# Kernel tuning notes

Measured on AMD Instinct MI355X. Metric: run time of the kernel, lower is better.

The kernel has to match this reference:

```python
import jax, jax.numpy as jnp
import numpy as np

N = 32768      # total nodes (2048 graphs * 16 nodes)
E = 491520     # total edges (2048 graphs * 16*15)
F = 11         # in_node_nf
H = 64         # hidden_nf
G = 2048       # number of graphs
NN = 16        # nodes per graph
R = 1024       # n_reactions
L = 4          # n_layers
EIN = 2 * H + 1        # edge_mlp input: [h[row], h[col], radial]
NIN = H + H + F        # node_mlp input: [h, agg, node_attr=h0]


def setup_inputs() -> dict:
    key = jax.random.key(0)
    ks = jax.random.split(key, 24)
    s = 0.05
    d = {
        "h0": jax.random.normal(ks[0], (N, F), jnp.float32),
        "positions": jax.random.normal(ks[1], (N, 3), jnp.float32),
        "edges": jax.random.randint(ks[2], (2, E), 0, N),
        "node_mask": jnp.ones((N, 1), jnp.float32),
        "edge_mask": jnp.ones((E, 1), jnp.float32),
        "reaction_indexes": jax.random.randint(ks[3], (G,), 0, R),
        "reaction_signs": jax.random.normal(ks[4], (G,), jnp.float32),
        # params
        "emb_w": jax.random.normal(ks[5], (F, H), jnp.float32) * s,
        "emb_b": jnp.zeros((H,), jnp.float32),
        "edge_w1": jax.random.normal(ks[6], (L, EIN, H), jnp.float32) * s,
        "edge_b1": jnp.zeros((L, H), jnp.float32),
        "edge_w2": jax.random.normal(ks[7], (L, H, H), jnp.float32) * s,
        "edge_b2": jnp.zeros((L, H), jnp.float32),
        "node_w1": jax.random.normal(ks[8], (L, NIN, H), jnp.float32) * s,
        "node_b1": jnp.zeros((L, H), jnp.float32),
        "node_w2": jax.random.normal(ks[9], (L, H, H), jnp.float32) * s,
        "node_b2": jnp.zeros((L, H), jnp.float32),
        "dec_w1": jax.random.normal(ks[10], (H, H), jnp.float32) * s,
        "dec_b1": jnp.zeros((H,), jnp.float32),
        "dec_w2": jax.random.normal(ks[11], (H, H), jnp.float32) * s,
        "dec_b2": jnp.zeros((H,), jnp.float32),
        "g_w1": jax.random.normal(ks[12], (H, H), jnp.float32) * s,
        "g_b1": jnp.zeros((H,), jnp.float32),
        "g_w2": jax.random.normal(ks[13], (H, 1), jnp.float32) * s,
        "g_b2": jnp.zeros((1,), jnp.float32),
        "n_nodes": NN,
        "n_reactions": R,
    }
    return d


def reference(h0, positions, edges, node_mask, edge_mask, reaction_indexes,
              reaction_signs, emb_w, emb_b, edge_w1, edge_b1, edge_w2, edge_b2,
              node_w1, node_b1, node_w2, node_b2, dec_w1, dec_b1, dec_w2,
              dec_b2, g_w1, g_b1, g_w2, g_b2, n_nodes, n_reactions):
    silu = jax.nn.silu
    row, col = edges[0], edges[1]
    n = h0.shape[0]

    # radial is constant across layers (coords never updated in this variant)
    coord_diff = positions[row] - positions[col]          # [E, 3]
    radial = jnp.sum(coord_diff ** 2, axis=1, keepdims=True)  # [E, 1]

    h = h0 @ emb_w + emb_b                                # [N, H]
    for i in range(edge_w1.shape[0]):
        # edge model
        e_in = jnp.concatenate([h[row], h[col], radial], axis=1)  # [E, 2H+1]
        e = silu(e_in @ edge_w1[i] + edge_b1[i])
        e = silu(e @ edge_w2[i] + edge_b2[i])             # [E, H]
        e = e * edge_mask
        # scatter-sum aggregation by source node
        agg = jax.ops.segment_sum(e, row, num_segments=n)  # [N, H]
        # node model (node_attr = h0)
        n_in = jnp.concatenate([h, agg, h0], axis=1)      # [N, 2H+F]
        h = silu(n_in @ node_w1[i] + node_b1[i]) @ node_w2[i] + node_b2[i]

    # node decoder
    h = silu(h @ dec_w1 + dec_b1) @ dec_w2 + dec_b2
    h = h * node_mask
    # pool per graph (fixed n_nodes per graph)
    hg = h.reshape(-1, n_nodes, h.shape[-1]).sum(axis=1)  # [G, H]
    # graph decoder
    temp = silu(hg @ g_w1 + g_b1) @ g_w2 + g_b2           # [G, 1]
    # signed per-reaction aggregation
    pred = jnp.zeros((n_reactions,), h.dtype).at[reaction_indexes].add(
        temp[:, 0] * reaction_signs)
    return pred
```

## Files before the change

### kernel.cpp

```cpp
#include <hip/hip_runtime.h>
#include <math.h>
#include <stdint.h>

#define N_NODES 32768
#define N_EDGES 491520
#define F_IN    11
#define H       64
#define G_GRAPHS 2048
#define NN_PER_G 16
#define R_REACT 1024
#define L_LAYERS 4
#define EIN     129
#define NIN     139
#define NPBLK   32

#define WPROJ 0
#define WE2   65536
#define WN1   98304
#define WN2   180224
#define WD1   212992
#define WD2   221184
#define WTOT  229376

typedef __attribute__((ext_vector_type(8))) short short8;
typedef __attribute__((ext_vector_type(4))) float f32x4;

__device__ __forceinline__ float silu_f(float x) {
    return x * __builtin_amdgcn_rcpf(1.0f + __expf(-x));
}
__device__ __forceinline__ void atomAddF(float* p, float v) {
    unsafeAtomicAdd(p, v);
}
__device__ __forceinline__ float bf2f(unsigned short b) {
    union { float f; unsigned u; } v; v.u = ((unsigned)b) << 16;
    return v.f;
}
__device__ __forceinline__ unsigned short f2bf(float x) {
    union { float f; unsigned u; } v; v.f = x;
    unsigned r = v.u + 0x7FFFu + ((v.u >> 16) & 1u);
    return (unsigned short)(r >> 16);
}
__device__ __forceinline__ void splitbf(float x, unsigned short& hi, unsigned short& lo) {
    hi = f2bf(x);
    lo = f2bf(x - bf2f(hi));
}
__device__ __forceinline__ void splitbf_t(float x, unsigned short& hi, unsigned short& lo) {
    union { float f; unsigned u; } v; v.f = x;
    hi = (unsigned short)(v.u >> 16);
    union { float f; unsigned u; } w; w.f = x - bf2f(hi);
    lo = (unsigned short)(w.u >> 16);
}

__global__ __launch_bounds__(64) void k_prepw(
        const float* __restrict__ ew1, const float* __restrict__ ew2,
        const float* __restrict__ nw1, const float* __restrict__ nw2,
        const float* __restrict__ dw1, const float* __restrict__ dw2,
        short* __restrict__ wsW) {
    const int b = blockIdx.x;
    const int lane = threadIdx.x;
    const int quad = lane >> 4, m16 = lane & 15;
    short8 h8, l8;
    short* base; int fidx, half;

    if (b < 64) {
        int l = b >> 4, f = b & 15;
        int nt = f >> 1, kf = f & 1;
#pragma unroll
        for (int j = 0; j < 8; ++j) {
            int row = (nt >= 4 ? 64 : 0) + kf * 32 + quad * 8 + j;
            unsigned short hi, lo;
            splitbf(ew1[l * EIN * H + row * H + (nt & 3) * 16 + m16], hi, lo);
            h8[j] = (short)hi; l8[j] = (short)lo;
        }
        base = wsW + WPROJ + l * 16384; fidx = f; half = 8192;
    } else if (b < 96) {
        int bb = b - 64; int l = bb >> 3, f = bb & 7;
        int nt = f >> 1, kf = f & 1;
#pragma unroll
        for (int j = 0; j < 8; ++j) {
            int row = kf * 32 + quad * 8 + j;
            unsigned short hi, lo;
            splitbf(ew2[l * H * H + row * H + nt * 16 + m16], hi, lo);
            h8[j] = (short)hi; l8[j] = (short)lo;
        }
        base = wsW + WE2 + l * 8192; fidx = f; half = 4096;
    } else if (b < 176) {
        int bb = b - 96; int l = bb / 20, f = bb % 20;
        int nt = f / 5, kf = f % 5;
#pragma unroll
        for (int j = 0; j < 8; ++j) {
            int row = kf * 32 + quad * 8 + j;
            float w = (row < NIN) ? nw1[l * NIN * H + row * H + nt * 16 + m16] : 0.0f;
            unsigned short hi, lo; splitbf(w, hi, lo);
            h8[j] = (short)hi; l8[j] = (short)lo;
        }
        base = wsW + WN1 + l * 20480; fidx = f; half = 10240;
    } else if (b < 208) {
        int bb = b - 176; int l = bb >> 3, f = bb & 7;
        int nt = f >> 1, kf = f & 1;
#pragma unroll
        for (int j = 0; j < 8; ++j) {
            int row = kf * 32 + quad * 8 + j;
            unsigned short hi, lo;
            splitbf(nw2[l * H * H + row * H + nt * 16 + m16], hi, lo);
            h8[j] = (short)hi; l8[j] = (short)lo;
        }
        base = wsW + WN2 + l * 8192; fidx = f; half = 4096;
    } else if (b < 216) {
        int f = b - 208;
        int nt = f >> 1, kf = f & 1;
#pragma unroll
        for (int j = 0; j < 8; ++j) {
            int row = kf * 32 + quad * 8 + j;
            unsigned short hi, lo;
            splitbf(dw1[row * H + nt * 16 + m16], hi, lo);
            h8[j] = (short)hi; l8[j] = (short)lo;
        }
        base = wsW + WD1; fidx = f; half = 4096;
    } else {
        int f = b - 216;
        int nt = f >> 1, kf = f & 1;
#pragma unroll
        for (int j = 0; j < 8; ++j) {
            int row = kf * 32 + quad * 8 + j;
            unsigned short hi, lo;
            splitbf(dw2[row * H + nt * 16 + m16], hi, lo);
            h8[j] = (short)hi; l8[j] = (short)lo;
        }
        base = wsW + WD2; fidx = f; half = 4096;
    }
    *(short8*)(base + (fidx * 64 + lane) * 8) = h8;
    *(short8*)(base + half + (fidx * 64 + lane) * 8) = l8;
}

__global__ __launch_bounds__(256) void k_embed(
        const float* __restrict__ h0, const float* __restrict__ emb_w,
        const float* __restrict__ emb_b, float* __restrict__ h) {
    int tid = blockIdx.x * 256 + threadIdx.x;
    int n = tid >> 6, j = tid & 63;
    float acc = emb_b[j];
#pragma unroll
    for (int k = 0; k < F_IN; ++k)
        acc += h0[n * F_IN + k] * emb_w[k * H + j];
    h[tid] = acc;
}

__global__ __launch_bounds__(256) void k_radial(
        const int* __restrict__ edges, const float* __restrict__ pos,
        float* __restrict__ radial) {
    int e = blockIdx.x * 256 + threadIdx.x;
    int r = edges[e], c = edges[N_EDGES + e];
    float dx = pos[r * 3 + 0] - pos[c * 3 + 0];
    float dy = pos[r * 3 + 1] - pos[c * 3 + 1];
    float dz = pos[r * 3 + 2] - pos[c * 3 + 2];
    radial[e] = dx * dx + dy * dy + dz * dz;
}

__global__ __launch_bounds__(256) void k_hist(
        const int* __restrict__ edges, int* __restrict__ deg) {
    int e = blockIdx.x * 256 + threadIdx.x;
    atomicAdd(&deg[edges[e]], 1);
}

__global__ __launch_bounds__(128) void k_scan_blk(
        const int* __restrict__ deg, int* __restrict__ off,
        int* __restrict__ bsum) {
    __shared__ int sd[128];
    int b = blockIdx.x;
    sd[threadIdx.x] = deg[b * 128 + threadIdx.x];
    __syncthreads();
    if (threadIdx.x == 0) {
        int s = 0;
        for (int i = 0; i < 128; ++i) { int d = sd[i]; sd[i] = s; s += d; }
        bsum[b] = s;
    }
    __syncthreads();
    off[b * 128 + threadIdx.x] = sd[threadIdx.x];
}

__global__ __launch_bounds__(256) void k_scan_top(
        const int* __restrict__ bsum, int* __restrict__ bbase) {
    __shared__ int sb[256];
    sb[threadIdx.x] = bsum[threadIdx.x];
    __syncthreads();
    if (threadIdx.x == 0) {
        int s = 0;
        for (int i = 0; i < 256; ++i) { int d = sb[i]; sb[i] = s; s += d; }
    }
    __syncthreads();
    bbase[threadIdx.x] = sb[threadIdx.x];
}

__global__ __launch_bounds__(256) void k_cursor(
        const int* __restrict__ off, const int* __restrict__ bbase,
        int* __restrict__ nstart, int* __restrict__ cursor) {
    int n = blockIdx.x * 256 + threadIdx.x;
    int ns = off[n] + bbase[n >> 7];
    nstart[n] = ns;
    cursor[n] = ns;
    if (n == 0) nstart[N_NODES] = N_EDGES;
}

__global__ __launch_bounds__(256) void k_fill(
        const int* __restrict__ edges, const float* __restrict__ radial,
        const float* __restrict__ emask, int* __restrict__ cursor,
        int* __restrict__ csrP, float* __restrict__ csrR,
        float* __restrict__ csrM) {
    int e = blockIdx.x * 256 + threadIdx.x;
    int r = edges[e];
    int pos = atomicAdd(&cursor[r], 1);
    csrP[pos] = edges[N_EDGES + e] | ((r & (NPBLK - 1)) << 16);
    csrR[pos] = radial[e];
    csrM[pos] = emask[e];
}

__global__ __launch_bounds__(64, 2) void k_nodeproj_m(
        const float* __restrict__ h, const short* __restrict__ wP,
        const float* __restrict__ b1,
        float* __restrict__ PA, float* __restrict__ PB) {
    const int lane = threadIdx.x;
    const int quad = lane >> 4, m16 = lane & 15;
    const int nb = blockIdx.x * 16;

    const float* hp = h + (nb + m16) * H + quad * 8;
    float av[16];
    *(float4*)&av[0]  = *(const float4*)(hp + 0);
    *(float4*)&av[4]  = *(const float4*)(hp + 4);
    *(float4*)&av[8]  = *(const float4*)(hp + 32);
    *(float4*)&av[12] = *(const float4*)(hp + 36);
    float b1v[4];
#pragma unroll
    for (int nt = 0; nt < 4; ++nt) b1v[nt] = b1[nt * 16 + m16];

    short8 Ah0, Ah1, Al0, Al1;
#pragma unroll
    for (int j = 0; j < 8; ++j) {
        unsigned short hi, lo;
        splitbf_t(av[j], hi, lo);     Ah0[j] = (short)hi; Al0[j] = (short)lo;
        splitbf_t(av[8 + j], hi, lo); Ah1[j] = (short)hi; Al1[j] = (short)lo;
    }
#pragma unroll
    for (int nt = 0; nt < 8; ++nt) {
        short8 bh0 = *(const short8*)(wP + ((nt*2+0) * 64 + lane) * 8);
        short8 bh1 = *(const short8*)(wP + ((nt*2+1) * 64 + lane) * 8);
        short8 bl0 = *(const short8*)(wP + 8192 + ((nt*2+0) * 64 + lane) * 8);
        short8 bl1 = *(const short8*)(wP + 8192 + ((nt*2+1) * 64 + lane) * 8);
        f32x4 a = {0.0f, 0.0f, 0.0f, 0.0f};
        a = __builtin_amdgcn_mfma_f32_16x16x32_bf16(Ah0, bh0, a, 0, 0, 0);
        a = __builtin_amdgcn_mfma_f32_16x16x32_bf16(Ah1, bh1, a, 0, 0, 0);
        a = __builtin_amdgcn_mfma_f32_16x16x32_bf16(Ah0, bl0, a, 0, 0, 0);
        a = __builtin_amdgcn_mfma_f32_16x16x32_bf16(Ah1, bl1, a, 0, 0, 0);
        a = __builtin_amdgcn_mfma_f32_16x16x32_bf16(Al0, bh0, a, 0, 0, 0);
        a = __builtin_amdgcn_mfma_f32_16x16x32_bf16(Al1, bh1, a, 0, 0, 0);
#pragma unroll
        for (int r4 = 0; r4 < 4; ++r4) {
            const int node = nb + quad * 4 + r4;
            if (nt < 4)
                PA[node * H + nt * 16 + m16] = a[r4] + b1v[nt];
            else
                PB[node * H + (nt - 4) * 16 + m16] = a[r4];
        }
    }
}

__global__ __launch_bounds__(256, 2) void k_edge6(
        const float* __restrict__ PA, const float* __restrict__ PB,
        const int* __restrict__ nstart, const int* __restrict__ csrP,
        const float* __restrict__ csrR, const float* __restrict__ csrM,
        const float* __restrict__ W1,
        const short* __restrict__ wE2, const float* __restrict__ b2,
        float* __restrict__ agg) {
    const int tid = threadIdx.x;
    const int lane = tid & 63, wave = tid >> 6;
    const int quad = lane >> 4, m16 = lane & 15;
    const int n0 = blockIdx.x * NPBLK;

    __shared__ float aggld[NPBLK * 68];
    for (int i = tid; i < NPBLK * 68; i += 256) aggld[i] = 0.0f;

    short8 Bh[8], Bl[8];
#pragma unroll
    for (int f = 0; f < 8; ++f) {
        Bh[f] = *(const short8*)(wE2 + (f * 64 + lane) * 8);
        Bl[f] = *(const short8*)(wE2 + 4096 + (f * 64 + lane) * 8);
    }
    float w1cr[16];
#pragma unroll
    for (int i = 0; i < 16; ++i) {
        int k = (i < 8) ? (quad * 8 + i) : (32 + quad * 8 + (i - 8));
        w1cr[i] = W1[128 * H + k];
    }
    float b2v[4];
#pragma unroll
    for (int nt = 0; nt < 4; ++nt) b2v[nt] = b2[nt * 16 + m16];

    const int start = nstart[n0];
    const int end   = nstart[n0 + NPBLK];
    __syncthreads();

    const int ntiles = (end - start + 15) >> 4;

    int   pkA = 0, pkB = 0;
    float radA = 0.0f, radB = 0.0f;
    float avA[16], bvA[16];

    int tA = wave;
    bool haveA = tA < ntiles;
    if (haveA) {
        const int idx = start + tA * 16 + m16;
        const int ss  = min(idx, N_EDGES - 1);
        pkA  = csrP[ss];
        radA = csrR[ss];
        const int c  = pkA & 0xFFFF;
        const int rl = pkA >> 16;
        const float* par = PA + (n0 + rl) * H + quad * 8;
        const float* pbr = PB + c * H + quad * 8;
        *(float4*)&avA[0]  = *(const float4*)(par + 0);
        *(float4*)&avA[4]  = *(const float4*)(par + 4);
        *(float4*)&avA[8]  = *(const float4*)(par + 32);
        *(float4*)&avA[12] = *(const float4*)(par + 36);
        *(float4*)&bvA[0]  = *(const float4*)(pbr + 0);
        *(float4*)&bvA[4]  = *(const float4*)(pbr + 4);
        *(float4*)&bvA[8]  = *(const float4*)(pbr + 32);
        *(float4*)&bvA[12] = *(const float4*)(pbr + 36);
    }
    int tB = tA + 4;
    bool haveB = tB < ntiles;
    if (haveB) {
        const int idx = start + tB * 16 + m16;
        const int ss  = min(idx, N_EDGES - 1);
        pkB  = csrP[ss];
        radB = csrR[ss];
    }

    while (haveA) {
        float bvB[16];
        if (haveB) {
            const int c = pkB & 0xFFFF;
            const float* pbr = PB + c * H + quad * 8;
            *(float4*)&bvB[0]  = *(const float4*)(pbr + 0);
            *(float4*)&bvB[4]  = *(const float4*)(pbr + 4);
            *(float4*)&bvB[8]  = *(const float4*)(pbr + 32);
            *(float4*)&bvB[12] = *(const float4*)(pbr + 36);
        }
        const int tC = tB + 4;
        const bool haveC = tC < ntiles;
        int pkC = 0; float radC = 0.0f;
        if (haveC) {
            const int idx = start + tC * 16 + m16;
            const int ss  = min(idx, N_EDGES - 1);
            pkC  = csrP[ss];
            radC = csrR[ss];
        }
        int rlq[4]; float mkq[4];
        const int sb = start + tA * 16 + quad * 4;
#pragma unroll
        for (int r4 = 0; r4 < 4; ++r4) {
            int s = sb + r4, s2 = min(s, N_EDGES - 1);
            rlq[r4] = csrP[s2] >> 16;
            mkq[r4] = (s < end) ? csrM[s2] : 0.0f;
        }

        short8 Ah0, Ah1, Al0, Al1;
#pragma unroll
        for (int i = 0; i < 8; ++i) {
            unsigned short hi, lo;
            splitbf_t(silu_f(avA[i] + bvA[i] + radA * w1cr[i]), hi, lo);
            Ah0[i] = (short)hi; Al0[i] = (short)lo;
            splitbf_t(silu_f(avA[8+i] + bvA[8+i] + radA * w1cr[8+i]), hi, lo);
            Ah1[i] = (short)hi; Al1[i] = (short)lo;
        }
        f32x4 acc[4];
#pragma unroll
        for (int nt = 0; nt < 4; ++nt) {
            f32x4 a = {0.0f, 0.0f, 0.0f, 0.0f};
            a = __builtin_amdgcn_mfma_f32_16x16x32_bf16(Ah0, Bh[nt*2+0], a, 0, 0, 0);
            a = __builtin_amdgcn_mfma_f32_16x16x32_bf16(Ah1, Bh[nt*2+1], a, 0, 0, 0);
            a = __builtin_amdgcn_mfma_f32_16x16x32_bf16(Ah0, Bl[nt*2+0], a, 0, 0, 0);
            a = __builtin_amdgcn_mfma_f32_16x16x32_bf16(Ah1, Bl[nt*2+1], a, 0, 0, 0);
            a = __builtin_amdgcn_mfma_f32_16x16x32_bf16(Al0, Bh[nt*2+0], a, 0, 0, 0);
            a = __builtin_amdgcn_mfma_f32_16x16x32_bf16(Al1, Bh[nt*2+1], a, 0, 0, 0);
            acc[nt] = a;
        }

#pragma unroll
        for (int nt = 0; nt < 4; ++nt) {
            float oo[4];
#pragma unroll
            for (int r4 = 0; r4 < 4; ++r4)
                oo[r4] = silu_f(acc[nt][r4] + b2v[nt]) * mkq[r4];
            int cur = rlq[0]; float s = oo[0];
#pragma unroll
            for (int r4 = 1; r4 < 4; ++r4) {
                if (rlq[r4] == cur) { s += oo[r4]; }
                else {
                    atomicAdd(&aggld[cur * 68 + nt * 16 + m16], s);
                    cur = rlq[r4]; s = oo[r4];
                }
            }
            atomicAdd(&aggld[cur * 68 + nt * 16 + m16], s);
        }

        if (haveB) {
            const int rl = pkB >> 16;
            const float* par = PA + (n0 + rl) * H + quad * 8;
            *(float4*)&avA[0]  = *(const float4*)(par + 0);
            *(float4*)&avA[4]  = *(const float4*)(par + 4);
            *(float4*)&avA[8]  = *(const float4*)(par + 32);
            *(float4*)&avA[12] = *(const float4*)(par + 36);
#pragma unroll
            for (int i = 0; i < 16; ++i) bvA[i] = bvB[i];
            pkA = pkB; radA = radB;
        }
        pkB = pkC; radB = radC;
        tA = tB; tB = tC; haveA = haveB; haveB = haveC;
    }

    __syncthreads();
#pragma unroll
    for (int i = tid; i < NPBLK * 16; i += 256) {
        int n = i >> 4, cb = (i & 15) << 2;
        *(float4*)&agg[(n0 + n) * H + cb] = *(const float4*)&aggld[n * 68 + cb];
    }
}

__global__ __launch_bounds__(64, 2) void k_node_m(
        float* __restrict__ h, const float* __restrict__ agg,
        const float* __restrict__ h0,
        const short* __restrict__ wN1, const float* __restrict__ b1,
        const short* __restrict__ wN2, const float* __restrict__ b2) {
    const int lane = threadIdx.x;
    const int quad = lane >> 4, m16 = lane & 15;
    const int nb = blockIdx.x * 16;

    float b1v[4], b2v[4];
#pragma unroll
    for (int nt = 0; nt < 4; ++nt) {
        b1v[nt] = b1[nt * 16 + m16];
        b2v[nt] = b2[nt * 16 + m16];
    }

    __shared__ float tld[16 * 68];

    float a1[5][8];
    const float* hp = h + (nb + m16) * H + quad * 8;
    const float* ap = agg + (nb + m16) * H + quad * 8;
    *(float4*)&a1[0][0] = *(const float4*)(hp + 0);
    *(float4*)&a1[0][4] = *(const float4*)(hp + 4);
    *(float4*)&a1[1][0] = *(const float4*)(hp + 32);
    *(float4*)&a1[1][4] = *(const float4*)(hp + 36);
    *(float4*)&a1[2][0] = *(const float4*)(ap + 0);
    *(float4*)&a1[2][4] = *(const float4*)(ap + 4);
    *(float4*)&a1[3][0] = *(const float4*)(ap + 32);
    *(float4*)&a1[3][4] = *(const float4*)(ap + 36);
    const float* h0p = h0 + (nb + m16) * F_IN;
#pragma unroll
    for (int j = 0; j < 8; ++j) {
        int kk = quad * 8 + j;
        a1[4][j] = (kk < F_IN) ? h0p[kk] : 0.0f;
    }
    short8 A1h[5], A1l[5];
#pragma unroll
    for (int kf = 0; kf < 5; ++kf) {
        short8 ah, al;
#pragma unroll
        for (int j = 0; j < 8; ++j) {
            unsigned short hi, lo; splitbf_t(a1[kf][j], hi, lo);
            ah[j] = (short)hi; al[j] = (short)lo;
        }
        A1h[kf] = ah; A1l[kf] = al;
    }
#pragma unroll
    for (int nt = 0; nt < 4; ++nt) {
        short8 bh[5], bl[5];
#pragma unroll
        for (int kf = 0; kf < 5; ++kf) {
            bh[kf] = *(const short8*)(wN1 + ((nt*5+kf) * 64 + lane) * 8);
            bl[kf] = *(const short8*)(wN1 + 10240 + ((nt*5+kf) * 64 + lane) * 8);
        }
        f32x4 a = {0.0f, 0.0f, 0.0f, 0.0f};
#pragma unroll
        for (int kf = 0; kf < 5; ++kf)
            a = __builtin_amdgcn_mfma_f32_16x16x32_bf16(A1h[kf], bh[kf], a, 0, 0, 0);
#pragma unroll
        for (int kf = 0; kf < 5; ++kf)
            a = __builtin_amdgcn_mfma_f32_16x16x32_bf16(A1h[kf], bl[kf], a, 0, 0, 0);
#pragma unroll
        for (int kf = 0; kf < 5; ++kf)
            a = __builtin_amdgcn_mfma_f32_16x16x32_bf16(A1l[kf], bh[kf], a, 0, 0, 0);
#pragma unroll
        for (int r4 = 0; r4 < 4; ++r4)
            tld[(quad * 4 + r4) * 68 + nt * 16 + m16] = silu_f(a[r4] + b1v[nt]);
    }
    __syncthreads();
    float a2[16];
    *(float4*)&a2[0]  = *(const float4*)&tld[m16 * 68 + quad * 8 + 0];
    *(float4*)&a2[4]  = *(const float4*)&tld[m16 * 68 + quad * 8 + 4];
    *(float4*)&a2[8]  = *(const float4*)&tld[m16 * 68 + quad * 8 + 32];
    *(float4*)&a2[12] = *(const float4*)&tld[m16 * 68 + quad * 8 + 36];
    short8 A2h0, A2h1, A2l0, A2l1;
#pragma unroll
    for (int j = 0; j < 8; ++j) {
        unsigned short hi, lo;
        splitbf_t(a2[j], hi, lo);     A2h0[j] = (short)hi; A2l0[j] = (short)lo;
        splitbf_t(a2[8+j], hi, lo);   A2h1[j] = (short)hi; A2l1[j] = (short)lo;
    }
#pragma unroll
    for (int nt = 0; nt < 4; ++nt) {
        short8 bh0 = *(const short8*)(wN2 + ((nt*2+0) * 64 + lane) * 8);
        short8 bh1 = *(const short8*)(wN2 + ((nt*2+1) * 64 + lane) * 8);
        short8 bl0 = *(const short8*)(wN2 + 4096 + ((nt*2+0) * 64 + lane) * 8);
        short8 bl1 = *(const short8*)(wN2 + 4096 + ((nt*2+1) * 64 + lane) * 8);
        f32x4 a = {0.0f, 0.0f, 0.0f, 0.0f};
        a = __builtin_amdgcn_mfma_f32_16x16x32_bf16(A2h0, bh0, a, 0, 0, 0);
        a = __builtin_amdgcn_mfma_f32_16x16x32_bf16(A2h1, bh1, a, 0, 0, 0);
        a = __builtin_amdgcn_mfma_f32_16x16x32_bf16(A2h0, bl0, a, 0, 0, 0);
        a = __builtin_amdgcn_mfma_f32_16x16x32_bf16(A2h1, bl1, a, 0, 0, 0);
        a = __builtin_amdgcn_mfma_f32_16x16x32_bf16(A2l0, bh0, a, 0, 0, 0);
        a = __builtin_amdgcn_mfma_f32_16x16x32_bf16(A2l1, bh1, a, 0, 0, 0);
#pragma unroll
        for (int r4 = 0; r4 < 4; ++r4) {
            const int node = nb + quad * 4 + r4;
            h[node * H + nt * 16 + m16] = a[r4] + b2v[nt];
        }
    }
}

__global__ __launch_bounds__(64, 2) void k_dec_m(
        float* __restrict__ h, const float* __restrict__ nmask,
        const short* __restrict__ wD1, const float* __restrict__ b1,
        const short* __restrict__ wD2, const float* __restrict__ b2) {
    const int lane = threadIdx.x;
    const int quad = lane >> 4, m16 = lane & 15;
    const int nb = blockIdx.x * 16;

    float b1v[4], b2v[4];
#pragma unroll
    for (int nt = 0; nt < 4; ++nt) {
        b1v[nt] = b1[nt * 16 + m16];
        b2v[nt] = b2[nt * 16 + m16];
    }
    __shared__ float tld[16 * 68];

    const float* hp = h + (nb + m16) * H + quad * 8;
    float av[16];
    *(float4*)&av[0]  = *(const float4*)(hp + 0);
    *(float4*)&av[4]  = *(const float4*)(hp + 4);
    *(float4*)&av[8]  = *(const float4*)(hp + 32);
    *(float4*)&av[12] = *(const float4*)(hp + 36);
    short8 Ah0, Ah1, Al0, Al1;
#pragma unroll
    for (int j = 0; j < 8; ++j) {
        unsigned short hi, lo;
        splitbf_t(av[j], hi, lo);     Ah0[j] = (short)hi; Al0[j] = (short)lo;
        splitbf_t(av[8+j], hi, lo);   Ah1[j] = (short)hi; Al1[j] = (short)lo;
    }
#pragma unroll
    for (int nt = 0; nt < 4; ++nt) {
        short8 bh0 = *(const short8*)(wD1 + ((nt*2+0) * 64 + lane) * 8);
        short8 bh1 = *(const short8*)(wD1 + ((nt*2+1) * 64 + lane) * 8);
        short8 bl0 = *(const short8*)(wD1 + 4096 + ((nt*2+0) * 64 + lane) * 8);
        short8 bl1 = *(const short8*)(wD1 + 4096 + ((nt*2+1) * 64 + lane) * 8);
        f32x4 a = {0.0f, 0.0f, 0.0f, 0.0f};
        a = __builtin_amdgcn_mfma_f32_16x16x32_bf16(Ah0, bh0, a, 0, 0, 0);
        a = __builtin_amdgcn_mfma_f32_16x16x32_bf16(Ah1, bh1, a, 0, 0, 0);
        a = __builtin_amdgcn_mfma_f32_16x16x32_bf16(Ah0, bl0, a, 0, 0, 0);
        a = __builtin_amdgcn_mfma_f32_16x16x32_bf16(Ah1, bl1, a, 0, 0, 0);
        a = __builtin_amdgcn_mfma_f32_16x16x32_bf16(Al0, bh0, a, 0, 0, 0);
        a = __builtin_amdgcn_mfma_f32_16x16x32_bf16(Al1, bh1, a, 0, 0, 0);
#pragma unroll
        for (int r4 = 0; r4 < 4; ++r4)
            tld[(quad * 4 + r4) * 68 + nt * 16 + m16] = silu_f(a[r4] + b1v[nt]);
    }
    __syncthreads();
    float a2[16];
    *(float4*)&a2[0]  = *(const float4*)&tld[m16 * 68 + quad * 8 + 0];
    *(float4*)&a2[4]  = *(const float4*)&tld[m16 * 68 + quad * 8 + 4];
    *(float4*)&a2[8]  = *(const float4*)&tld[m16 * 68 + quad * 8 + 32];
    *(float4*)&a2[12] = *(const float4*)&tld[m16 * 68 + quad * 8 + 36];
    short8 A2h0, A2h1, A2l0, A2l1;
#pragma unroll
    for (int j = 0; j < 8; ++j) {
        unsigned short hi, lo;
        splitbf_t(a2[j], hi, lo);     A2h0[j] = (short)hi; A2l0[j] = (short)lo;
        splitbf_t(a2[8+j], hi, lo);   A2h1[j] = (short)hi; A2l1[j] = (short)lo;
    }
#pragma unroll
    for (int nt = 0; nt < 4; ++nt) {
        short8 bh0 = *(const short8*)(wD2 + ((nt*2+0) * 64 + lane) * 8);
        short8 bh1 = *(const short8*)(wD2 + ((nt*2+1) * 64 + lane) * 8);
        short8 bl0 = *(const short8*)(wD2 + 4096 + ((nt*2+0) * 64 + lane) * 8);
        short8 bl1 = *(const short8*)(wD2 + 4096 + ((nt*2+1) * 64 + lane) * 8);
        f32x4 a = {0.0f, 0.0f, 0.0f, 0.0f};
        a = __builtin_amdgcn_mfma_f32_16x16x32_bf16(A2h0, bh0, a, 0, 0, 0);
        a = __builtin_amdgcn_mfma_f32_16x16x32_bf16(A2h1, bh1, a, 0, 0, 0);
        a = __builtin_amdgcn_mfma_f32_16x16x32_bf16(A2h0, bl0, a, 0, 0, 0);
        a = __builtin_amdgcn_mfma_f32_16x16x32_bf16(A2h1, bl1, a, 0, 0, 0);
        a = __builtin_amdgcn_mfma_f32_16x16x32_bf16(A2l0, bh0, a, 0, 0, 0);
        a = __builtin_amdgcn_mfma_f32_16x16x32_bf16(A2l1, bh1, a, 0, 0, 0);
#pragma unroll
        for (int r4 = 0; r4 < 4; ++r4) {
            const int node = nb + quad * 4 + r4;
            const float nm = nmask[node];
            h[node * H + nt * 16 + m16] = (a[r4] + b2v[nt]) * nm;
        }
    }
}

__global__ __launch_bounds__(64) void k_graph(
        const float* __restrict__ h, const int* __restrict__ rid,
        const float* __restrict__ rsign,
        const float* __restrict__ W1, const float* __restrict__ b1,
        const float* __restrict__ W2, const float* __restrict__ b2,
        float* __restrict__ pred) {
    const int g = blockIdx.x;
    const int lane = threadIdx.x;
    float hgv = 0.0f;
#pragma unroll
    for (int m = 0; m < NN_PER_G; ++m)
        hgv += h[(g * NN_PER_G + m) * H + lane];
    __shared__ __align__(16) float hgs[64];
    hgs[lane] = hgv;
    __syncthreads();
    float acc = b1[lane];
#pragma unroll
    for (int k = 0; k < H; ++k)
        acc += hgs[k] * W1[k * H + lane];
    float part = silu_f(acc) * W2[lane];
#pragma unroll
    for (int off = 32; off > 0; off >>= 1)
        part += __shfl_down(part, off);
    if (lane == 0)
        atomAddF(&pred[rid[g]], (part + b2[0]) * rsign[g]);
}

extern "C" void kernel_launch(void* const* d_in, const int* in_sizes, int n_in,
                              void* d_out, int out_size, void* d_ws, size_t ws_size,
                              hipStream_t stream) {
    const float* h0      = (const float*)d_in[0];
    const float* pos     = (const float*)d_in[1];
    const int*   edges   = (const int*)d_in[2];
    const float* nmask   = (const float*)d_in[3];
    const float* emask   = (const float*)d_in[4];
    const int*   rid     = (const int*)d_in[5];
    const float* rsign   = (const float*)d_in[6];
    const float* emb_w   = (const float*)d_in[7];
    const float* emb_b   = (const float*)d_in[8];
    const float* edge_w1 = (const float*)d_in[9];
    const float* edge_b1 = (const float*)d_in[10];
    const float* edge_w2 = (const float*)d_in[11];
    const float* edge_b2 = (const float*)d_in[12];
    const float* node_w1 = (const float*)d_in[13];
    const float* node_b1 = (const float*)d_in[14];
    const float* node_w2 = (const float*)d_in[15];
    const float* node_b2 = (const float*)d_in[16];
    const float* dec_w1  = (const float*)d_in[17];
    const float* dec_b1  = (const float*)d_in[18];
    const float* dec_w2  = (const float*)d_in[19];
    const float* dec_b2  = (const float*)d_in[20];
    const float* g_w1    = (const float*)d_in[21];
    const float* g_b1    = (const float*)d_in[22];
    const float* g_w2    = (const float*)d_in[23];
    const float* g_b2    = (const float*)d_in[24];

    float* h      = (float*)d_ws;
    float* agg    = h + N_NODES * H;
    float* radial = agg + N_NODES * H;
    float* PA     = radial + N_EDGES;
    float* PB     = PA + N_NODES * H;
    float* csrR   = PB + N_NODES * H;
    float* csrM   = csrR + N_EDGES;
    int*   csrP   = (int*)(csrM + N_EDGES);
    int*   deg    = csrP + N_EDGES;
    int*   off    = deg + N_NODES;
    int*   bsum   = off + N_NODES;
    int*   bbase  = bsum + 256;
    int*   nstart = bbase + 256;
    int*   cursor = nstart + N_NODES + 1;
    short* wsW    = (short*)((((uintptr_t)(cursor + N_NODES)) + 255) & ~(uintptr_t)255);
    float* pred   = (float*)d_out;

    hipMemsetAsync(d_out, 0, R_REACT * sizeof(float), stream);
    hipMemsetAsync(deg, 0, N_NODES * sizeof(int), stream);

    k_prepw<<<224, 64, 0, stream>>>(edge_w1, edge_w2, node_w1, node_w2,
                                    dec_w1, dec_w2, wsW);
    k_embed<<<(N_NODES * H) / 256, 256, 0, stream>>>(h0, emb_w, emb_b, h);
    k_radial<<<N_EDGES / 256, 256, 0, stream>>>(edges, pos, radial);
    k_hist<<<N_EDGES / 256, 256, 0, stream>>>(edges, deg);
    k_scan_blk<<<256, 128, 0, stream>>>(deg, off, bsum);
    k_scan_top<<<1, 256, 0, stream>>>(bsum, bbase);
    k_cursor<<<N_NODES / 256, 256, 0, stream>>>(off, bbase, nstart, cursor);
    k_fill<<<N_EDGES / 256, 256, 0, stream>>>(edges, radial, emask, cursor,
                                              csrP, csrR, csrM);

    for (int i = 0; i < L_LAYERS; ++i) {
        k_nodeproj_m<<<N_NODES / 16, 64, 0, stream>>>(
            h, wsW + WPROJ + i * 16384, edge_b1 + i * H, PA, PB);
        k_edge6<<<N_NODES / NPBLK, 256, 0, stream>>>(
            PA, PB, nstart, csrP, csrR, csrM,
            edge_w1 + i * EIN * H,
            wsW + WE2 + i * 8192, edge_b2 + i * H, agg);
        k_node_m<<<N_NODES / 16, 64, 0, stream>>>(
            h, agg, h0,
            wsW + WN1 + i * 20480, node_b1 + i * H,
            wsW + WN2 + i * 8192,  node_b2 + i * H);
    }
    k_dec_m<<<N_NODES / 16, 64, 0, stream>>>(h, nmask, wsW + WD1, dec_b1,
                                             wsW + WD2, dec_b2);
    k_graph<<<G_GRAPHS, 64, 0, stream>>>(h, rid, rsign, g_w1, g_b1, g_w2,
                                         g_b2, pred);
}
```

Measured before the change: 524.9 us.

## Fuse embed, node MLP, edge projection, decoder and graph pooling into fewer kernels

Folds the embedding into an MFMA kernel that also computes the first edge projection, and folds the node MLP of each layer together with the next layer's edge projection. The last layer's node MLP is merged with the node decoder, the per-graph pooling and the graph MLP, and radial computation moves into the CSR fill kernel. The aim is to cut kernel launches and the global round trips of h and radial. NPBLK also drops from 32 to 16, which doubles the edge kernel's block count, and the merged kernels use more registers and extra barriers.

```diff
diff --git a/kernel.cpp b/kernel.cpp
--- a/kernel.cpp
+++ b/kernel.cpp
@@ -12,7 +12,7 @@
 #define L_LAYERS 4
 #define EIN     129
 #define NIN     139
-#define NPBLK   32
+#define NPBLK   16
 
 #define WPROJ 0
 #define WE2   65536
@@ -20,7 +20,8 @@
 #define WN2   180224
 #define WD1   212992
 #define WD2   221184
-#define WTOT  229376
+#define WEMB  229376
+#define WTOT  233472
 
 typedef __attribute__((ext_vector_type(8))) short short8;
 typedef __attribute__((ext_vector_type(4))) float f32x4;
@@ -55,6 +56,7 @@
         const float* __restrict__ ew1, const float* __restrict__ ew2,
         const float* __restrict__ nw1, const float* __restrict__ nw2,
         const float* __restrict__ dw1, const float* __restrict__ dw2,
+        const float* __restrict__ embw,
         short* __restrict__ wsW) {
     const int b = blockIdx.x;
     const int lane = threadIdx.x;
@@ -117,7 +119,7 @@
             h8[j] = (short)hi; l8[j] = (short)lo;
         }
         base = wsW + WD1; fidx = f; half = 4096;
-    } else {
+    } else if (b < 224) {
         int f = b - 216;
         int nt = f >> 1, kf = f & 1;
 #pragma unroll
@@ -128,32 +130,19 @@
             h8[j] = (short)hi; l8[j] = (short)lo;
         }
         base = wsW + WD2; fidx = f; half = 4096;
+    } else {
+        int f = b - 224;
+#pragma unroll
+        for (int j = 0; j < 8; ++j) {
+            int row = quad * 8 + j;
+            float w = (row < F_IN) ? embw[row * H + f * 16 + m16] : 0.0f;
+            unsigned short hi, lo; splitbf(w, hi, lo);
+            h8[j] = (short)hi; l8[j] = (short)lo;
+        }
+        base = wsW + WEMB; fidx = f; half = 2048;
     }
     *(short8*)(base + (fidx * 64 + lane) * 8) = h8;
     *(short8*)(base + half + (fidx * 64 + lane) * 8) = l8;
-}
-
-__global__ __launch_bounds__(256) void k_embed(
-        const float* __restrict__ h0, const float* __restrict__ emb_w,
-        const float* __restrict__ emb_b, float* __restrict__ h) {
-    int tid = blockIdx.x * 256 + threadIdx.x;
-    int n = tid >> 6, j = tid & 63;
-    float acc = emb_b[j];
-#pragma unroll
-    for (int k = 0; k < F_IN; ++k)
-        acc += h0[n * F_IN + k] * emb_w[k * H + j];
-    h[tid] = acc;
-}
-
-__global__ __launch_bounds__(256) void k_radial(
-        const int* __restrict__ edges, const float* __restrict__ pos,
-        float* __restrict__ radial) {
-    int e = blockIdx.x * 256 + threadIdx.x;
-    int r = edges[e], c = edges[N_EDGES + e];
-    float dx = pos[r * 3 + 0] - pos[c * 3 + 0];
-    float dy = pos[r * 3 + 1] - pos[c * 3 + 1];
-    float dz = pos[r * 3 + 2] - pos[c * 3 + 2];
-    radial[e] = dx * dx + dy * dy + dz * dz;
 }
 
 __global__ __launch_bounds__(256) void k_hist(
@@ -202,36 +191,71 @@
 }
 
 __global__ __launch_bounds__(256) void k_fill(
-        const int* __restrict__ edges, const float* __restrict__ radial,
+        const int* __restrict__ edges, const float* __restrict__ posi,
         const float* __restrict__ emask, int* __restrict__ cursor,
         int* __restrict__ csrP, float* __restrict__ csrR,
         float* __restrict__ csrM) {
     int e = blockIdx.x * 256 + threadIdx.x;
-    int r = edges[e];
-    int pos = atomicAdd(&cursor[r], 1);
-    csrP[pos] = edges[N_EDGES + e] | ((r & (NPBLK - 1)) << 16);
-    csrR[pos] = radial[e];
-    csrM[pos] = emask[e];
-}
-
-__global__ __launch_bounds__(64, 2) void k_nodeproj_m(
-        const float* __restrict__ h, const short* __restrict__ wP,
-        const float* __restrict__ b1,
-        float* __restrict__ PA, float* __restrict__ PB) {
+    int r = edges[e], c = edges[N_EDGES + e];
+    float dx = posi[r * 3 + 0] - posi[c * 3 + 0];
+    float dy = posi[r * 3 + 1] - posi[c * 3 + 1];
+    float dz = posi[r * 3 + 2] - posi[c * 3 + 2];
+    float rad = dx * dx + dy * dy + dz * dz;
+    int p = atomicAdd(&cursor[r], 1);
+    csrP[p] = c | ((r & (NPBLK - 1)) << 16);
+    csrR[p] = rad;
+    csrM[p] = emask[e];
+}
+
+__global__ __launch_bounds__(64, 2) void k_embed_proj(
+        const float* __restrict__ h0, const short* __restrict__ wEmb,
+        const float* __restrict__ emb_b,
+        const short* __restrict__ wP, const float* __restrict__ eb1,
+        float* __restrict__ h, float* __restrict__ PA, float* __restrict__ PB) {
     const int lane = threadIdx.x;
     const int quad = lane >> 4, m16 = lane & 15;
     const int nb = blockIdx.x * 16;
-
-    const float* hp = h + (nb + m16) * H + quad * 8;
+    __shared__ float tld[16 * 68];
+
+    float a0[8];
+    const float* h0p = h0 + (nb + m16) * F_IN;
+#pragma unroll
+    for (int j = 0; j < 8; ++j) {
+        int kk = quad * 8 + j;
+        a0[j] = (kk < F_IN) ? h0p[kk] : 0.0f;
+    }
+    short8 A0h, A0l;
+#pragma unroll
+    for (int j = 0; j < 8; ++j) {
+        unsigned short hi, lo; splitbf_t(a0[j], hi, lo);
+        A0h[j] = (short)hi; A0l[j] = (short)lo;
+    }
+    float ebv[4];
+#pragma unroll
+    for (int nt = 0; nt < 4; ++nt) ebv[nt] = emb_b[nt * 16 + m16];
+
+#pragma unroll
+    for (int nt = 0; nt < 4; ++nt) {
+        short8 bh = *(const short8*)(wEmb + (nt * 64 + lane) * 8);
+        short8 bl = *(const short8*)(wEmb + 2048 + (nt * 64 + lane) * 8);
+        f32x4 a = {0.0f, 0.0f, 0.0f, 0.0f};
+        a = __builtin_amdgcn_mfma_f32_16x16x32_bf16(A0h, bh, a, 0, 0, 0);
+        a = __builtin_amdgcn_mfma_f32_16x16x32_bf16(A0h, bl, a, 0, 0, 0);
+        a = __builtin_amdgcn_mfma_f32_16x16x32_bf16(A0l, bh, a, 0, 0, 0);
+#pragma unroll
+        for (int r4 = 0; r4 < 4; ++r4) {
+            const int node = nb + quad * 4 + r4;
+            float hv = a[r4] + ebv[nt];
+            h[node * H + nt * 16 + m16] = hv;
+            tld[(quad * 4 + r4) * 68 + nt * 16 + m16] = hv;
+        }
+    }
+    __syncthreads();
     float av[16];
-    *(float4*)&av[0]  = *(const float4*)(hp + 0);
-    *(float4*)&av[4]  = *(const float4*)(hp + 4);
-    *(float4*)&av[8]  = *(const float4*)(hp + 32);
-    *(float4*)&av[12] = *(const float4*)(hp + 36);
-    float b1v[4];
-#pragma unroll
-    for (int nt = 0; nt < 4; ++nt) b1v[nt] = b1[nt * 16 + m16];
-
+    *(float4*)&av[0]  = *(const float4*)&tld[m16 * 68 + quad * 8 + 0];
+    *(float4*)&av[4]  = *(const float4*)&tld[m16 * 68 + quad * 8 + 4];
+    *(float4*)&av[8]  = *(const float4*)&tld[m16 * 68 + quad * 8 + 32];
+    *(float4*)&av[12] = *(const float4*)&tld[m16 * 68 + quad * 8 + 36];
     short8 Ah0, Ah1, Al0, Al1;
 #pragma unroll
     for (int j = 0; j < 8; ++j) {
@@ -239,6 +263,9 @@
         splitbf_t(av[j], hi, lo);     Ah0[j] = (short)hi; Al0[j] = (short)lo;
         splitbf_t(av[8 + j], hi, lo); Ah1[j] = (short)hi; Al1[j] = (short)lo;
     }
+    float b1v[4];
+#pragma unroll
+    for (int nt = 0; nt < 4; ++nt) b1v[nt] = eb1[nt * 16 + m16];
 #pragma unroll
     for (int nt = 0; nt < 8; ++nt) {
         short8 bh0 = *(const short8*)(wP + ((nt*2+0) * 64 + lane) * 8);
@@ -424,11 +451,13 @@
     }
 }
 
-__global__ __launch_bounds__(64, 2) void k_node_m(
+__global__ __launch_bounds__(64, 2) void k_node_proj(
         float* __restrict__ h, const float* __restrict__ agg,
         const float* __restrict__ h0,
         const short* __restrict__ wN1, const float* __restrict__ b1,
-        const short* __restrict__ wN2, const float* __restrict__ b2) {
+        const short* __restrict__ wN2, const float* __restrict__ b2,
+        const short* __restrict__ wPn, const float* __restrict__ eb1n,
+        float* __restrict__ PA, float* __restrict__ PB) {
     const int lane = threadIdx.x;
     const int quad = lane >> 4, m16 = lane & 15;
     const int nb = blockIdx.x * 16;
@@ -439,7 +468,6 @@
         b1v[nt] = b1[nt * 16 + m16];
         b2v[nt] = b2[nt * 16 + m16];
     }
-
     __shared__ float tld[16 * 68];
 
     float a1[5][8];
@@ -505,6 +533,7 @@
         splitbf_t(a2[j], hi, lo);     A2h0[j] = (short)hi; A2l0[j] = (short)lo;
         splitbf_t(a2[8+j], hi, lo);   A2h1[j] = (short)hi; A2l1[j] = (short)lo;
     }
+    __syncthreads();
 #pragma unroll
     for (int nt = 0; nt < 4; ++nt) {
         short8 bh0 = *(const short8*)(wN2 + ((nt*2+0) * 64 + lane) * 8);
@@ -521,53 +550,128 @@
 #pragma unroll
         for (int r4 = 0; r4 < 4; ++r4) {
             const int node = nb + quad * 4 + r4;
-            h[node * H + nt * 16 + m16] = a[r4] + b2v[nt];
-        }
-    }
-}
-
-__global__ __launch_bounds__(64, 2) void k_dec_m(
-        float* __restrict__ h, const float* __restrict__ nmask,
-        const short* __restrict__ wD1, const float* __restrict__ b1,
-        const short* __restrict__ wD2, const float* __restrict__ b2) {
+            float hv = a[r4] + b2v[nt];
+            h[node * H + nt * 16 + m16] = hv;
+            tld[(quad * 4 + r4) * 68 + nt * 16 + m16] = hv;
+        }
+    }
+    __syncthreads();
+    float av[16];
+    *(float4*)&av[0]  = *(const float4*)&tld[m16 * 68 + quad * 8 + 0];
+    *(float4*)&av[4]  = *(const float4*)&tld[m16 * 68 + quad * 8 + 4];
+    *(float4*)&av[8]  = *(const float4*)&tld[m16 * 68 + quad * 8 + 32];
+    *(float4*)&av[12] = *(const float4*)&tld[m16 * 68 + quad * 8 + 36];
+    short8 Ph0, Ph1, Pl0, Pl1;
+#pragma unroll
+    for (int j = 0; j < 8; ++j) {
+        unsigned short hi, lo;
+        splitbf_t(av[j], hi, lo);     Ph0[j] = (short)hi; Pl0[j] = (short)lo;
+        splitbf_t(av[8+j], hi, lo);   Ph1[j] = (short)hi; Pl1[j] = (short)lo;
+    }
+    float b1ev[4];
+#pragma unroll
+    for (int nt = 0; nt < 4; ++nt) b1ev[nt] = eb1n[nt * 16 + m16];
+#pragma unroll
+    for (int nt = 0; nt < 8; ++nt) {
+        short8 bh0 = *(const short8*)(wPn + ((nt*2+0) * 64 + lane) * 8);
+        short8 bh1 = *(const short8*)(wPn + ((nt*2+1) * 64 + lane) * 8);
+        short8 bl0 = *(const short8*)(wPn + 8192 + ((nt*2+0) * 64 + lane) * 8);
+        short8 bl1 = *(const short8*)(wPn + 8192 + ((nt*2+1) * 64 + lane) * 8);
+        f32x4 a = {0.0f, 0.0f, 0.0f, 0.0f};
+        a = __builtin_amdgcn_mfma_f32_16x16x32_bf16(Ph0, bh0, a, 0, 0, 0);
+        a = __builtin_amdgcn_mfma_f32_16x16x32_bf16(Ph1, bh1, a, 0, 0, 0);
+        a = __builtin_amdgcn_mfma_f32_16x16x32_bf16(Ph0, bl0, a, 0, 0, 0);
+        a = __builtin_amdgcn_mfma_f32_16x16x32_bf16(Ph1, bl1, a, 0, 0, 0);
+        a = __builtin_amdgcn_mfma_f32_16x16x32_bf16(Pl0, bh0, a, 0, 0, 0);
+        a = __builtin_amdgcn_mfma_f32_16x16x32_bf16(Pl1, bh1, a, 0, 0, 0);
+#pragma unroll
+        for (int r4 = 0; r4 < 4; ++r4) {
+            const int node = nb + quad * 4 + r4;
+            if (nt < 4)
+                PA[node * H + nt * 16 + m16] = a[r4] + b1ev[nt];
+            else
+                PB[node * H + (nt - 4) * 16 + m16] = a[r4];
+        }
+    }
+}
+
+__global__ __launch_bounds__(64, 2) void k_node_dec_graph(
+        const float* __restrict__ h, const float* __restrict__ agg,
+        const float* __restrict__ h0,
+        const short* __restrict__ wN1, const float* __restrict__ b1,
+        const short* __restrict__ wN2, const float* __restrict__ b2,
+        const short* __restrict__ wD1, const float* __restrict__ db1,
+        const short* __restrict__ wD2, const float* __restrict__ db2,
+        const float* __restrict__ nmask,
+        const float* __restrict__ gW1, const float* __restrict__ gb1,
+        const float* __restrict__ gW2, const float* __restrict__ gb2,
+        const int* __restrict__ rid, const float* __restrict__ rsign,
+        float* __restrict__ pred) {
     const int lane = threadIdx.x;
     const int quad = lane >> 4, m16 = lane & 15;
     const int nb = blockIdx.x * 16;
 
-    float b1v[4], b2v[4];
+    float b1v[4], b2v[4], db1v[4], db2v[4];
 #pragma unroll
     for (int nt = 0; nt < 4; ++nt) {
-        b1v[nt] = b1[nt * 16 + m16];
-        b2v[nt] = b2[nt * 16 + m16];
-    }
+        b1v[nt]  = b1[nt * 16 + m16];
+        b2v[nt]  = b2[nt * 16 + m16];
+        db1v[nt] = db1[nt * 16 + m16];
+        db2v[nt] = db2[nt * 16 + m16];
+    }
+    float nm[4];
+#pragma unroll
+    for (int r4 = 0; r4 < 4; ++r4) nm[r4] = nmask[nb + quad * 4 + r4];
+
     __shared__ float tld[16 * 68];
-
+    __shared__ __align__(16) float hgs[64];
+
+    float a1[5][8];
     const float* hp = h + (nb + m16) * H + quad * 8;
-    float av[16];
-    *(float4*)&av[0]  = *(const float4*)(hp + 0);
-    *(float4*)&av[4]  = *(const float4*)(hp + 4);
-    *(float4*)&av[8]  = *(const float4*)(hp + 32);
-    *(float4*)&av[12] = *(const float4*)(hp + 36);
-    short8 Ah0, Ah1, Al0, Al1;
-#pragma unroll
-    for (int j = 0; j < 8; ++j) {
-        unsigned short hi, lo;
-        splitbf_t(av[j], hi, lo);     Ah0[j] = (short)hi; Al0[j] = (short)lo;
-        splitbf_t(av[8+j], hi, lo);   Ah1[j] = (short)hi; Al1[j] = (short)lo;
+    const float* ap = agg + (nb + m16) * H + quad * 8;
+    *(float4*)&a1[0][0] = *(const float4*)(hp + 0);
+    *(float4*)&a1[0][4] = *(const float4*)(hp + 4);
+    *(float4*)&a1[1][0] = *(const float4*)(hp + 32);
+    *(float4*)&a1[1][4] = *(const float4*)(hp + 36);
+    *(float4*)&a1[2][0] = *(const float4*)(ap + 0);
+    *(float4*)&a1[2][4] = *(const float4*)(ap + 4);
+    *(float4*)&a1[3][0] = *(const float4*)(ap + 32);
+    *(float4*)&a1[3][4] = *(const float4*)(ap + 36);
+    const float* h0p = h0 + (nb + m16) * F_IN;
+#pragma unroll
+    for (int j = 0; j < 8; ++j) {
+        int kk = quad * 8 + j;
+        a1[4][j] = (kk < F_IN) ? h0p[kk] : 0.0f;
+    }
+    short8 A1h[5], A1l[5];
+#pragma unroll
+    for (int kf = 0; kf < 5; ++kf) {
+        short8 ah, al;
+#pragma unroll
+        for (int j = 0; j < 8; ++j) {
+            unsigned short hi, lo; splitbf_t(a1[kf][j], hi, lo);
+            ah[j] = (short)hi; al[j] = (short)lo;
+        }
+        A1h[kf] = ah; A1l[kf] = al;
     }
 #pragma unroll
     for (int nt = 0; nt < 4; ++nt) {
-        short8 bh0 = *(const short8*)(wD1 + ((nt*2+0) * 64 + lane) * 8);
-        short8 bh1 = *(const short8*)(wD1 + ((nt*2+1) * 64 + lane) * 8);
-        short8 bl0 = *(const short8*)(wD1 + 4096 + ((nt*2+0) * 64 + lane) * 8);
-        short8 bl1 = *(const short8*)(wD1 + 4096 + ((nt*2+1) * 64 + lane) * 8);
+        short8 bh[5], bl[5];
+#pragma unroll
+        for (int kf = 0; kf < 5; ++kf) {
+            bh[kf] = *(const short8*)(wN1 + ((nt*5+kf) * 64 + lane) * 8);
+            bl[kf] = *(const short8*)(wN1 + 10240 + ((nt*5+kf) * 64 + lane) * 8);
+        }
         f32x4 a = {0.0f, 0.0f, 0.0f, 0.0f};
-        a = __builtin_amdgcn_mfma_f32_16x16x32_bf16(Ah0, bh0, a, 0, 0, 0);
-        a = __builtin_amdgcn_mfma_f32_16x16x32_bf16(Ah1, bh1, a, 0, 0, 0);
-        a = __builtin_amdgcn_mfma_f32_16x16x32_bf16(Ah0, bl0, a, 0, 0, 0);
-        a = __builtin_amdgcn_mfma_f32_16x16x32_bf16(Ah1, bl1, a, 0, 0, 0);
-        a = __builtin_amdgcn_mfma_f32_16x16x32_bf16(Al0, bh0, a, 0, 0, 0);
-        a = __builtin_amdgcn_mfma_f32_16x16x32_bf16(Al1, bh1, a, 0, 0, 0);
+#pragma unroll
+        for (int kf = 0; kf < 5; ++kf)
+            a = __builtin_amdgcn_mfma_f32_16x16x32_bf16(A1h[kf], bh[kf], a, 0, 0, 0);
+#pragma unroll
+        for (int kf = 0; kf < 5; ++kf)
+            a = __builtin_amdgcn_mfma_f32_16x16x32_bf16(A1h[kf], bl[kf], a, 0, 0, 0);
+#pragma unroll
+        for (int kf = 0; kf < 5; ++kf)
+            a = __builtin_amdgcn_mfma_f32_16x16x32_bf16(A1l[kf], bh[kf], a, 0, 0, 0);
 #pragma unroll
         for (int r4 = 0; r4 < 4; ++r4)
             tld[(quad * 4 + r4) * 68 + nt * 16 + m16] = silu_f(a[r4] + b1v[nt]);
@@ -585,12 +689,13 @@
         splitbf_t(a2[j], hi, lo);     A2h0[j] = (short)hi; A2l0[j] = (short)lo;
         splitbf_t(a2[8+j], hi, lo);   A2h1[j] = (short)hi; A2l1[j] = (short)lo;
     }
+    __syncthreads();
 #pragma unroll
     for (int nt = 0; nt < 4; ++nt) {
-        short8 bh0 = *(const short8*)(wD2 + ((nt*2+0) * 64 + lane) * 8);
-        short8 bh1 = *(const short8*)(wD2 + ((nt*2+1) * 64 + lane) * 8);
-        short8 bl0 = *(const short8*)(wD2 + 4096 + ((nt*2+0) * 64 + lane) * 8);
-        short8 bl1 = *(const short8*)(wD2 + 4096 + ((nt*2+1) * 64 + lane) * 8);
+        short8 bh0 = *(const short8*)(wN2 + ((nt*2+0) * 64 + lane) * 8);
+        short8 bh1 = *(const short8*)(wN2 + ((nt*2+1) * 64 + lane) * 8);
+        short8 bl0 = *(const short8*)(wN2 + 4096 + ((nt*2+0) * 64 + lane) * 8);
+        short8 bl1 = *(const short8*)(wN2 + 4096 + ((nt*2+1) * 64 + lane) * 8);
         f32x4 a = {0.0f, 0.0f, 0.0f, 0.0f};
         a = __builtin_amdgcn_mfma_f32_16x16x32_bf16(A2h0, bh0, a, 0, 0, 0);
         a = __builtin_amdgcn_mfma_f32_16x16x32_bf16(A2h1, bh1, a, 0, 0, 0);
@@ -599,39 +704,85 @@
         a = __builtin_amdgcn_mfma_f32_16x16x32_bf16(A2l0, bh0, a, 0, 0, 0);
         a = __builtin_amdgcn_mfma_f32_16x16x32_bf16(A2l1, bh1, a, 0, 0, 0);
 #pragma unroll
-        for (int r4 = 0; r4 < 4; ++r4) {
-            const int node = nb + quad * 4 + r4;
-            const float nm = nmask[node];
-            h[node * H + nt * 16 + m16] = (a[r4] + b2v[nt]) * nm;
-        }
-    }
-}
-
-__global__ __launch_bounds__(64) void k_graph(
-        const float* __restrict__ h, const int* __restrict__ rid,
-        const float* __restrict__ rsign,
-        const float* __restrict__ W1, const float* __restrict__ b1,
-        const float* __restrict__ W2, const float* __restrict__ b2,
-        float* __restrict__ pred) {
-    const int g = blockIdx.x;
-    const int lane = threadIdx.x;
-    float hgv = 0.0f;
-#pragma unroll
-    for (int m = 0; m < NN_PER_G; ++m)
-        hgv += h[(g * NN_PER_G + m) * H + lane];
-    __shared__ __align__(16) float hgs[64];
-    hgs[lane] = hgv;
-    __syncthreads();
-    float acc = b1[lane];
+        for (int r4 = 0; r4 < 4; ++r4)
+            tld[(quad * 4 + r4) * 68 + nt * 16 + m16] = a[r4] + b2v[nt];
+    }
+    __syncthreads();
+    float av[16];
+    *(float4*)&av[0]  = *(const float4*)&tld[m16 * 68 + quad * 8 + 0];
+    *(float4*)&av[4]  = *(const float4*)&tld[m16 * 68 + quad * 8 + 4];
+    *(float4*)&av[8]  = *(const float4*)&tld[m16 * 68 + quad * 8 + 32];
+    *(float4*)&av[12] = *(const float4*)&tld[m16 * 68 + quad * 8 + 36];
+    short8 Dh0, Dh1, Dl0, Dl1;
+#pragma unroll
+    for (int j = 0; j < 8; ++j) {
+        unsigned short hi, lo;
+        splitbf_t(av[j], hi, lo);     Dh0[j] = (short)hi; Dl0[j] = (short)lo;
+        splitbf_t(av[8+j], hi, lo);   Dh1[j] = (short)hi; Dl1[j] = (short)lo;
+    }
+    __syncthreads();
+#pragma unroll
+    for (int nt = 0; nt < 4; ++nt) {
+        short8 bh0 = *(const short8*)(wD1 + ((nt*2+0) * 64 + lane) * 8);
+        short8 bh1 = *(const short8*)(wD1 + ((nt*2+1) * 64 + lane) * 8);
+        short8 bl0 = *(const short8*)(wD1 + 4096 + ((nt*2+0) * 64 + lane) * 8);
+        short8 bl1 = *(const short8*)(wD1 + 4096 + ((nt*2+1) * 64 + lane) * 8);
+        f32x4 a = {0.0f, 0.0f, 0.0f, 0.0f};
+        a = __builtin_amdgcn_mfma_f32_16x16x32_bf16(Dh0, bh0, a, 0, 0, 0);
+        a = __builtin_amdgcn_mfma_f32_16x16x32_bf16(Dh1, bh1, a, 0, 0, 0);
+        a = __builtin_amdgcn_mfma_f32_16x16x32_bf16(Dh0, bl0, a, 0, 0, 0);
+        a = __builtin_amdgcn_mfma_f32_16x16x32_bf16(Dh1, bl1, a, 0, 0, 0);
+        a = __builtin_amdgcn_mfma_f32_16x16x32_bf16(Dl0, bh0, a, 0, 0, 0);
+        a = __builtin_amdgcn_mfma_f32_16x16x32_bf16(Dl1, bh1, a, 0, 0, 0);
+#pragma unroll
+        for (int r4 = 0; r4 < 4; ++r4)
+            tld[(quad * 4 + r4) * 68 + nt * 16 + m16] = silu_f(a[r4] + db1v[nt]);
+    }
+    __syncthreads();
+    float a3[16];
+    *(float4*)&a3[0]  = *(const float4*)&tld[m16 * 68 + quad * 8 + 0];
+    *(float4*)&a3[4]  = *(const float4*)&tld[m16 * 68 + quad * 8 + 4];
+    *(float4*)&a3[8]  = *(const float4*)&tld[m16 * 68 + quad * 8 + 32];
+    *(float4*)&a3[12] = *(const float4*)&tld[m16 * 68 + quad * 8 + 36];
+    short8 Eh0, Eh1, El0, El1;
+#pragma unroll
+    for (int j = 0; j < 8; ++j) {
+        unsigned short hi, lo;
+        splitbf_t(a3[j], hi, lo);     Eh0[j] = (short)hi; El0[j] = (short)lo;
+        splitbf_t(a3[8+j], hi, lo);   Eh1[j] = (short)hi; El1[j] = (short)lo;
+    }
+#pragma unroll
+    for (int nt = 0; nt < 4; ++nt) {
+        short8 bh0 = *(const short8*)(wD2 + ((nt*2+0) * 64 + lane) * 8);
+        short8 bh1 = *(const short8*)(wD2 + ((nt*2+1) * 64 + lane) * 8);
+        short8 bl0 = *(const short8*)(wD2 + 4096 + ((nt*2+0) * 64 + lane) * 8);
+        short8 bl1 = *(const short8*)(wD2 + 4096 + ((nt*2+1) * 64 + lane) * 8);
+        f32x4 a = {0.0f, 0.0f, 0.0f, 0.0f};
+        a = __builtin_amdgcn_mfma_f32_16x16x32_bf16(Eh0, bh0, a, 0, 0, 0);
+        a = __builtin_amdgcn_mfma_f32_16x16x32_bf16(Eh1, bh1, a, 0, 0, 0);
+        a = __builtin_amdgcn_mfma_f32_16x16x32_bf16(Eh0, bl0, a, 0, 0, 0);
+        a = __builtin_amdgcn_mfma_f32_16x16x32_bf16(Eh1, bl1, a, 0, 0, 0);
+        a = __builtin_amdgcn_mfma_f32_16x16x32_bf16(El0, bh0, a, 0, 0, 0);
+        a = __builtin_amdgcn_mfma_f32_16x16x32_bf16(El1, bh1, a, 0, 0, 0);
+        float s = 0.0f;
+#pragma unroll
+        for (int r4 = 0; r4 < 4; ++r4)
+            s += (a[r4] + db2v[nt]) * nm[r4];
+        s += __shfl_xor(s, 16);
+        s += __shfl_xor(s, 32);
+        if (quad == 0) hgs[nt * 16 + m16] = s;
+    }
+    __syncthreads();
+    float acc = gb1[lane];
 #pragma unroll
     for (int k = 0; k < H; ++k)
-        acc += hgs[k] * W1[k * H + lane];
-    float part = silu_f(acc) * W2[lane];
+        acc += hgs[k] * gW1[k * H + lane];
+    float part = silu_f(acc) * gW2[lane];
 #pragma unroll
     for (int off = 32; off > 0; off >>= 1)
         part += __shfl_down(part, off);
     if (lane == 0)
-        atomAddF(&pred[rid[g]], (part + b2[0]) * rsign[g]);
+        atomAddF(&pred[rid[blockIdx.x]], (part + gb2[0]) * rsign[blockIdx.x]);
 }
 
 extern "C" void kernel_launch(void* const* d_in, const int* in_sizes, int n_in,
@@ -665,8 +816,7 @@
 
     float* h      = (float*)d_ws;
     float* agg    = h + N_NODES * H;
-    float* radial = agg + N_NODES * H;
-    float* PA     = radial + N_EDGES;
+    float* PA     = agg + N_NODES * H;
     float* PB     = PA + N_NODES * H;
     float* csrR   = PB + N_NODES * H;
     float* csrM   = csrR + N_EDGES;
@@ -683,31 +833,36 @@
     hipMemsetAsync(d_out, 0, R_REACT * sizeof(float), stream);
     hipMemsetAsync(deg, 0, N_NODES * sizeof(int), stream);
 
-    k_prepw<<<224, 64, 0, stream>>>(edge_w1, edge_w2, node_w1, node_w2,
-                                    dec_w1, dec_w2, wsW);
-    k_embed<<<(N_NODES * H) / 256, 256, 0, stream>>>(h0, emb_w, emb_b, h);
-    k_radial<<<N_EDGES / 256, 256, 0, stream>>>(edges, pos, radial);
+    k_prepw<<<228, 64, 0, stream>>>(edge_w1, edge_w2, node_w1, node_w2,
+                                    dec_w1, dec_w2, emb_w, wsW);
     k_hist<<<N_EDGES / 256, 256, 0, stream>>>(edges, deg);
     k_scan_blk<<<256, 128, 0, stream>>>(deg, off, bsum);
     k_scan_top<<<1, 256, 0, stream>>>(bsum, bbase);
     k_cursor<<<N_NODES / 256, 256, 0, stream>>>(off, bbase, nstart, cursor);
-    k_fill<<<N_EDGES / 256, 256, 0, stream>>>(edges, radial, emask, cursor,
+    k_fill<<<N_EDGES / 256, 256, 0, stream>>>(edges, pos, emask, cursor,
                                               csrP, csrR, csrM);
+    k_embed_proj<<<N_NODES / 16, 64, 0, stream>>>(
+        h0, wsW + WEMB, emb_b, wsW + WPROJ, edge_b1, h, PA, PB);
 
     for (int i = 0; i < L_LAYERS; ++i) {
-        k_nodeproj_m<<<N_NODES / 16, 64, 0, stream>>>(
-            h, wsW + WPROJ + i * 16384, edge_b1 + i * H, PA, PB);
         k_edge6<<<N_NODES / NPBLK, 256, 0, stream>>>(
             PA, PB, nstart, csrP, csrR, csrM,
             edge_w1 + i * EIN * H,
             wsW + WE2 + i * 8192, edge_b2 + i * H, agg);
-        k_node_m<<<N_NODES / 16, 64, 0, stream>>>(
-            h, agg, h0,
-            wsW + WN1 + i * 20480, node_b1 + i * H,
-            wsW + WN2 + i * 8192,  node_b2 + i * H);
-    }
-    k_dec_m<<<N_NODES / 16, 64, 0, stream>>>(h, nmask, wsW + WD1, dec_b1,
-                                             wsW + WD2, dec_b2);
-    k_graph<<<G_GRAPHS, 64, 0, stream>>>(h, rid, rsign, g_w1, g_b1, g_w2,
-                                         g_b2, pred);
-}
+        if (i < L_LAYERS - 1) {
+            k_node_proj<<<N_NODES / 16, 64, 0, stream>>>(
+                h, agg, h0,
+                wsW + WN1 + i * 20480, node_b1 + i * H,
+                wsW + WN2 + i * 8192,  node_b2 + i * H,
+                wsW + WPROJ + (i + 1) * 16384, edge_b1 + (i + 1) * H,
+                PA, PB);
+        } else {
+            k_node_dec_graph<<<N_NODES / 16, 64, 0, stream>>>(
+                h, agg, h0,
+                wsW + WN1 + i * 20480, node_b1 + i * H,
+                wsW + WN2 + i * 8192,  node_b2 + i * H,
+                wsW + WD1, dec_b1, wsW + WD2, dec_b2,
+                nmask, g_w1, g_b1, g_w2, g_b2, rid, rsign, pred);
+        }
+    }
+}
```

Result: faster. 482.8 us (-8.0%).
